# Performance work log

Hardware: AMD Instinct MI355X
Metric: run time of the kernel (lower is better)

Reference implementation:

```python
import jax, jax.numpy as jnp
import numpy as np

B, C, L, D, P = 64, 64, 720, 512, 336
P2, H = P // 2, 512  # H = hidden width of the ProbG branch


def setup_inputs() -> dict:
    key = jax.random.key(0)
    ks = jax.random.split(key, 20)
    def w(k, i, o):
        return jax.random.normal(k, (i, o), jnp.float32) / np.sqrt(i)
    return {
        "x_bsd": jax.random.normal(ks[0], (B, L, C), jnp.float32),
        "z0": jax.random.normal(ks[1], (B, C, D), jnp.float32),
        "y0": jax.random.normal(ks[2], (B, C, P), jnp.float32),
        # ProbG hidden branch (HID_GIVEN_X_V0 -> SS_Z_GIVEN_X_V0)
        "W_h": w(ks[3], L, H),
        "W_ssz": w(ks[4], H, 2 * D),
        # x->z scale/shift flows (versions v2..v5)
        "W_xz_v2": w(ks[5], L, 2 * D),
        "W_xz_v3": w(ks[6], L, 2 * D),
        "W_xz_v4": w(ks[7], L, 2 * D),
        "W_xz_v5": w(ks[8], L, 2 * D),
        # z->x scale/shift flows (v0, v2, v3, v5)
        "W_zx_v0": w(ks[9], D, 2 * L),
        "W_zx_v2": w(ks[10], D, 2 * L),
        "W_zx_v3": w(ks[11], D, 2 * L),
        "W_zx_v5": w(ks[12], D, 2 * L),
        # z->y scale/shift flow (v4, used inside encoding)
        "W_zy_v4": w(ks[13], D, 2 * P),
        # decode heads: ROT_IN_Y_V1 and KOO_Y_GIVEN_Z_V0
        "W_rot": w(ks[14], D, P2),
        "W_koo": w(ks[15], D, 2 * P),
        # Koopman complex params for y-space (a + i b per channel/pair)
        "a_y": jnp.ones((C, P2), jnp.float32),
        "b_y": jnp.zeros((C, P2), jnp.float32) + 0.1,
    }


def _ss(params):
    """Split conditioner output into (positive scale, shift)."""
    s_raw, t = jnp.split(params, 2, axis=-1)
    return jnp.exp(jnp.tanh(s_raw)), t


def _affine(v, cond, W):
    """Scale/shift flow: v <- v * s(cond) + t(cond)."""
    s, t = _ss(jnp.einsum('bck,km->bcm', cond, W))
    return v * s + t


def _rot(u, theta, inv=False):
    """Rotate interleaved (re, im) pairs of u [B,C,P] by angles theta [B,C,P/2]."""
    re, im = u[..., 0::2], u[..., 1::2]
    th = -theta if inv else theta
    c, s = jnp.cos(th), jnp.sin(th)
    return jnp.stack([c * re - s * im, s * re + c * im], axis=-1).reshape(u.shape)


def _koop(u, a, b, inv=False):
    """Koopman unit-complex multiply on interleaved pairs; a,b [C,P/2]."""
    n = jnp.sqrt(a * a + b * b)
    ca, cb = a / n, b / n
    cb = -cb if inv else cb
    re, im = u[..., 0::2], u[..., 1::2]
    return jnp.stack([ca * re - cb * im, cb * re + ca * im], axis=-1).reshape(u.shape)


def reference(x_bsd, z0, y0, W_h, W_ssz, W_xz_v2, W_xz_v3, W_xz_v4, W_xz_v5,
              W_zx_v0, W_zx_v2, W_zx_v3, W_zx_v5, W_zy_v4, W_rot, W_koo, a_y, b_y):
    x = jnp.transpose(x_bsd, (0, 2, 1))  # [B,C,L]
    z = z0 * 0.1                          # [B,C,D]
    y = y0 * 0.1                          # [B,C,P]
    # ---- encoding phase ----
    h = jax.nn.gelu(jnp.einsum('bcl,lk->bck', x, W_h))  # X_to_Z_PROB hidden
    z = _affine(z, h, W_ssz)
    x = _affine(x, z, W_zx_v0)
    z = _affine(z, x, W_xz_v2); x = _affine(x, z, W_zx_v2)
    z = _affine(z, x, W_xz_v3); x = _affine(x, z, W_zx_v3)
    z = _affine(z, x, W_xz_v4); y = _affine(y, z, W_zy_v4)  # Z_to_Y_V4
    z = _affine(z, x, W_xz_v5); x = _affine(x, z, W_zx_v5)
    pre_y = y
    # ---- decode: rotate -> ky -> scale -> ky.inv -> rot.inv -> shift ----
    theta = jnp.pi * jnp.tanh(jnp.einsum('bcd,dp->bcp', z, W_rot))   # [B,C,P/2]
    scale, shift = _ss(jnp.einsum('bcd,dp->bcp', z, W_koo))          # [B,C,P]
    const = _koop(_rot(pre_y, theta), a_y, b_y)
    accu = const * scale
    accu = _rot(_koop(accu, a_y, b_y, inv=True), theta, inv=True) + shift
    return jnp.transpose(accu, (0, 2, 1))  # [B,P,C]
```

## Files before the change

### kernel.cpp

```cpp
#include <hip/hip_runtime.h>
#include <hip/hip_bf16.h>
#include <math.h>

#define BB  64
#define CC  64
#define LL  720
#define LLP 736
#define DD  512
#define PP  336
#define P2C 168
#define HH  512
#define MM  (BB*CC)

typedef _Float16 f16x8 __attribute__((ext_vector_type(8)));
typedef float    f32x4 __attribute__((ext_vector_type(4)));

#define GLDS16(g, l) __builtin_amdgcn_global_load_lds( \
    (const __attribute__((address_space(1))) void*)(g), \
    (__attribute__((address_space(3))) void*)(l), 16, 0, 0)

struct WDesc { const float* src; _Float16* dstHi; _Float16* dstLo;
               int K, N, Kpad, tbase, tilesN; };
struct WTab  { WDesc d[12]; };

__global__ __launch_bounds__(256) void k_convert(WTab tab) {
  __shared__ float tile[16][17];
  const int bid = blockIdx.x;
  int wi = 0;
#pragma unroll
  for (int i = 1; i < 12; ++i) if (bid >= tab.d[i].tbase) wi = i;
  const WDesc d = tab.d[wi];
  const int lt = bid - d.tbase;
  const int tk = lt / d.tilesN, tn = lt % d.tilesN;
  const int k0 = tk * 16, n0 = tn * 16;
  const int tx = threadIdx.x & 15, ty = threadIdx.x >> 4;
  float v = 0.f;
  if (n0 + tx < d.N) v = d.src[(size_t)(k0 + ty) * d.N + n0 + tx];
  tile[ty][tx] = v;
  __syncthreads();
  if (n0 + ty < d.N) {
    const float w = tile[tx][ty];
    const _Float16 h = (_Float16)w;
    const _Float16 l = (_Float16)(w - (float)h);
    const size_t base = (size_t)(n0 + ty) * d.Kpad;
    d.dstHi[base + k0 + tx] = h;
    d.dstLo[base + k0 + tx] = l;
    if (d.Kpad != d.K && k0 + 16 == d.K) {
      d.dstHi[base + d.K + tx] = (_Float16)0.f;
      d.dstLo[base + d.K + tx] = (_Float16)0.f;
    }
  }
}

__global__ __launch_bounds__(256) void k_xpose(const float* __restrict__ xbsd,
                                               _Float16* __restrict__ xhi,
                                               _Float16* __restrict__ xlo) {
  __shared__ float tile[16][17];
  const int b = blockIdx.z, l0 = blockIdx.x * 16, c0 = blockIdx.y * 16;
  const int tx = threadIdx.x, ty = threadIdx.y;
  tile[ty][tx] = xbsd[(size_t)b * LL * CC + (size_t)(l0 + ty) * CC + c0 + tx];
  __syncthreads();
  const float v = tile[tx][ty];
  const _Float16 h = (_Float16)v;
  const _Float16 l = (_Float16)(v - (float)h);
  const size_t m = (size_t)b * CC + c0 + ty;
  xhi[m * LLP + l0 + tx] = h;
  xlo[m * LLP + l0 + tx] = l;
  if (l0 == 704) {
    xhi[m * LLP + 720 + tx] = (_Float16)0.f;
    xlo[m * LLP + 720 + tx] = (_Float16)0.f;
  }
}

template<int EPI, bool DUAL, bool VIN16, bool OUT_T>
__global__ __launch_bounds__(256)
void k_gemm(const _Float16* Ahi, const _Float16* Alo, int lda,
            const _Float16* Whi, const _Float16* Wlo, int ldw,
            const float* Vin32, const _Float16* VinHi,
            const _Float16* VinLo, int ldv, float vscale,
            float* outT32,
            _Float16* outHi, _Float16* outLo, int ldo,
            int Kp, int Nv) {
  constexpr int NB   = DUAL ? 128 : 64;
  constexpr int ABUF = 64 * 32;
  constexpr int BBUF = NB * 32;
  constexpr int NCH  = 8 + 2 * (NB / 16);
  constexpr int NCHW = NCH / 4;
  __shared__ _Float16 smem[2 * ABUF + 2 * BBUF];

  const int m0 = blockIdx.y * 64;
  const int n0 = blockIdx.x * 64;
  const int tid = threadIdx.x;
  const int w = tid >> 6, lane = tid & 63, q = lane >> 4, r = lane & 15;
  const int wr = (w & 1) * 32, wc = (w >> 1) * 32;
  const int lr = lane >> 2, ls = lane & 3;

  f32x4 accS[2][2] = {};
  f32x4 accT[2][2] = {};

  const int nk = Kp >> 5;
  for (int kc = 0; kc < nk; ++kc) {
    const int k0 = kc << 5;
#pragma unroll
    for (int cc = 0; cc < NCHW; ++cc) {
      const int chunk = w * NCHW + cc;
      const _Float16* gsrc;
      _Float16* ldst;
      if (chunk < 4) {
        const int rb = chunk * 16;
        const int R = rb + lr;
        const int ss = ls ^ ((R >> 1) & 3);
        gsrc = Ahi + (size_t)(m0 + R) * lda + k0 + ss * 8;
        ldst = smem + rb * 32;
      } else if (chunk < 8) {
        const int rb = (chunk - 4) * 16;
        const int R = rb + lr;
        const int ss = ls ^ ((R >> 1) & 3);
        gsrc = Alo + (size_t)(m0 + R) * lda + k0 + ss * 8;
        ldst = smem + ABUF + rb * 32;
      } else if (chunk < 8 + NB / 16) {
        const int rb = (chunk - 8) * 16;
        const int R = rb + lr;
        const int ss = ls ^ ((R >> 1) & 3);
        const int wrow = (R < 64) ? (n0 + R) : (Nv + n0 + (R - 64));
        gsrc = Whi + (size_t)wrow * ldw + k0 + ss * 8;
        ldst = smem + 2 * ABUF + rb * 32;
      } else {
        const int rb = (chunk - 8 - NB / 16) * 16;
        const int R = rb + lr;
        const int ss = ls ^ ((R >> 1) & 3);
        const int wrow = (R < 64) ? (n0 + R) : (Nv + n0 + (R - 64));
        gsrc = Wlo + (size_t)wrow * ldw + k0 + ss * 8;
        ldst = smem + 2 * ABUF + BBUF + rb * 32;
      }
      GLDS16(gsrc, ldst);
    }
    __syncthreads();

    f16x8 ah[2], al[2];
#pragma unroll
    for (int rt = 0; rt < 2; ++rt) {
      const int R = wr + rt * 16 + r;
      const int t = (q ^ ((R >> 1) & 3)) * 8;
      ah[rt] = *(const f16x8*)(smem + R * 32 + t);
      al[rt] = *(const f16x8*)(smem + ABUF + R * 32 + t);
    }
#pragma unroll
    for (int ct = 0; ct < 2; ++ct) {
      const int RB = wc + ct * 16 + r;
      const int tb = (q ^ ((RB >> 1) & 3)) * 8;
      const f16x8 bh = *(const f16x8*)(smem + 2 * ABUF + RB * 32 + tb);
      const f16x8 bl = *(const f16x8*)(smem + 2 * ABUF + BBUF + RB * 32 + tb);
#pragma unroll
      for (int rt = 0; rt < 2; ++rt) {
        accS[rt][ct] = __builtin_amdgcn_mfma_f32_16x16x32_f16(ah[rt], bh, accS[rt][ct], 0, 0, 0);
        accS[rt][ct] = __builtin_amdgcn_mfma_f32_16x16x32_f16(al[rt], bh, accS[rt][ct], 0, 0, 0);
        accS[rt][ct] = __builtin_amdgcn_mfma_f32_16x16x32_f16(ah[rt], bl, accS[rt][ct], 0, 0, 0);
      }
      if (DUAL) {
        const int RT = 64 + RB;
        const int tt = (q ^ ((RT >> 1) & 3)) * 8;
        const f16x8 chh = *(const f16x8*)(smem + 2 * ABUF + RT * 32 + tt);
        const f16x8 cll = *(const f16x8*)(smem + 2 * ABUF + BBUF + RT * 32 + tt);
#pragma unroll
        for (int rt = 0; rt < 2; ++rt) {
          accT[rt][ct] = __builtin_amdgcn_mfma_f32_16x16x32_f16(ah[rt], chh, accT[rt][ct], 0, 0, 0);
          accT[rt][ct] = __builtin_amdgcn_mfma_f32_16x16x32_f16(al[rt], chh, accT[rt][ct], 0, 0, 0);
          accT[rt][ct] = __builtin_amdgcn_mfma_f32_16x16x32_f16(ah[rt], cll, accT[rt][ct], 0, 0, 0);
        }
      }
    }
    __syncthreads();
  }

#pragma unroll
  for (int rt = 0; rt < 2; ++rt) {
    const int mb = m0 + wr + rt * 16 + q * 4;
#pragma unroll
    for (int ct = 0; ct < 2; ++ct) {
      const int n = n0 + wc + ct * 16 + r;
      if (n >= Nv) continue;
      if (EPI == 2) {
        *(f32x4*)(outT32 + (size_t)n * MM + mb) = accS[rt][ct];
      } else if (EPI == 1) {
#pragma unroll
        for (int g = 0; g < 4; ++g) {
          const int m = mb + g;
          const float v = accS[rt][ct][g];
          const float o = 0.5f * v * (1.0f + tanhf(0.7978845608028654f * (v + 0.044715f * v * v * v)));
          const _Float16 h = (_Float16)o;
          outHi[(size_t)m * ldo + n] = h;
          outLo[(size_t)m * ldo + n] = (_Float16)(o - (float)h);
        }
      } else {
        f32x4 o;
#pragma unroll
        for (int g = 0; g < 4; ++g) {
          const int m = mb + g;
          float v;
          if (VIN16) {
            v = (float)VinHi[(size_t)m * ldv + n] + (float)VinLo[(size_t)m * ldv + n];
          } else {
            v = Vin32[(size_t)m * ldv + n];
          }
          const float s = expf(tanhf(accS[rt][ct][g]));
          o[g] = v * vscale * s + accT[rt][ct][g];
        }
        if (OUT_T) {
          *(f32x4*)(outT32 + (size_t)n * MM + mb) = o;
        } else {
#pragma unroll
          for (int g = 0; g < 4; ++g) {
            const int m = mb + g;
            const _Float16 h = (_Float16)o[g];
            outHi[(size_t)m * ldo + n] = h;
            outLo[(size_t)m * ldo + n] = (_Float16)(o[g] - (float)h);
          }
        }
      }
    }
  }
}

__global__ __launch_bounds__(256) void k_final(const float* __restrict__ Pt,
                                               const float* __restrict__ yT,
                                               const float* __restrict__ Ay,
                                               const float* __restrict__ By,
                                               float* __restrict__ out) {
  const int c = threadIdx.x;
  const int j = blockIdx.x * 4 + threadIdx.y;
  const int b = blockIdx.y;
  const int m = b * 64 + c;
  const float th = 3.14159265358979323846f * tanhf(Pt[(size_t)j * MM + m]);
  const float sc0 = expf(tanhf(Pt[(size_t)(168 + 2 * j) * MM + m]));
  const float sc1 = expf(tanhf(Pt[(size_t)(169 + 2 * j) * MM + m]));
  const float t0 = Pt[(size_t)(504 + 2 * j) * MM + m];
  const float t1 = Pt[(size_t)(505 + 2 * j) * MM + m];
  const float re = yT[(size_t)(2 * j) * MM + m];
  const float im = yT[(size_t)(2 * j + 1) * MM + m];
  const float a = Ay[c * P2C + j], bb = By[c * P2C + j];
  const float rn = rsqrtf(a * a + bb * bb);
  const float ca = a * rn, cb = bb * rn;
  float s1v, c1;
  sincosf(th, &s1v, &c1);
  const float r1 = c1 * re - s1v * im, i1 = s1v * re + c1 * im;
  const float r2 = ca * r1 - cb * i1,  i2 = cb * r1 + ca * i1;
  const float r3 = r2 * sc0,           i3 = i2 * sc1;
  const float r4 = ca * r3 + cb * i3,  i4 = ca * i3 - cb * r3;
  const float r5 = c1 * r4 + s1v * i4, i5 = c1 * i4 - s1v * r4;
  out[(size_t)b * PP * CC + (size_t)(2 * j) * CC + c]     = r5 + t0;
  out[(size_t)b * PP * CC + (size_t)(2 * j + 1) * CC + c] = i5 + t1;
}

extern "C" void kernel_launch(void* const* d_in, const int* in_sizes, int n_in,
                              void* d_out, int out_size, void* d_ws, size_t ws_size,
                              hipStream_t stream) {
  const float* x_bsd   = (const float*)d_in[0];
  const float* z0      = (const float*)d_in[1];
  const float* y0      = (const float*)d_in[2];
  const float* W_h     = (const float*)d_in[3];
  const float* W_ssz   = (const float*)d_in[4];
  const float* W_xz_v2 = (const float*)d_in[5];
  const float* W_xz_v3 = (const float*)d_in[6];
  const float* W_xz_v4 = (const float*)d_in[7];
  const float* W_xz_v5 = (const float*)d_in[8];
  const float* W_zx_v0 = (const float*)d_in[9];
  const float* W_zx_v2 = (const float*)d_in[10];
  const float* W_zx_v3 = (const float*)d_in[11];
  const float* W_zy_v4 = (const float*)d_in[13];
  const float* W_rot   = (const float*)d_in[14];
  const float* W_koo   = (const float*)d_in[15];
  const float* a_y     = (const float*)d_in[16];
  const float* b_y     = (const float*)d_in[17];
  float* out = (float*)d_out;

  char* p = (char*)d_ws;
  auto alloc = [&](size_t bytes) -> void* {
    void* r = (void*)p; p += (bytes + 255) & ~(size_t)255; return r;
  };
  float*    yT  = (float*)alloc((size_t)PP * MM * 4);
  float*    Pt  = (float*)alloc((size_t)(P2C * 5) * MM * 4);
  _Float16* xhi = (_Float16*)alloc((size_t)MM * LLP * 2);
  _Float16* xlo = (_Float16*)alloc((size_t)MM * LLP * 2);
  _Float16* zhi = (_Float16*)alloc((size_t)MM * DD * 2);
  _Float16* zlo = (_Float16*)alloc((size_t)MM * DD * 2);
  _Float16* hhi = (_Float16*)alloc((size_t)MM * HH * 2);
  _Float16* hlo = (_Float16*)alloc((size_t)MM * HH * 2);
  auto wpair = [&](size_t elems, _Float16** lo) -> _Float16* {
    _Float16* hi = (_Float16*)alloc(elems * 2);
    *lo = (_Float16*)alloc(elems * 2);
    return hi;
  };
  _Float16 *tWhL, *tWsszL, *tWxz2L, *tWxz3L, *tWxz4L, *tWxz5L;
  _Float16 *tWzx0L, *tWzx2L, *tWzx3L, *tWzyL, *tWcatL;
  _Float16* tWh   = wpair((size_t)HH * LLP, &tWhL);
  _Float16* tWssz = wpair((size_t)(2*DD) * DD, &tWsszL);
  _Float16* tWxz2 = wpair((size_t)(2*DD) * LLP, &tWxz2L);
  _Float16* tWxz3 = wpair((size_t)(2*DD) * LLP, &tWxz3L);
  _Float16* tWxz4 = wpair((size_t)(2*DD) * LLP, &tWxz4L);
  _Float16* tWxz5 = wpair((size_t)(2*DD) * LLP, &tWxz5L);
  _Float16* tWzx0 = wpair((size_t)1536 * DD, &tWzx0L);
  _Float16* tWzx2 = wpair((size_t)1536 * DD, &tWzx2L);
  _Float16* tWzx3 = wpair((size_t)1536 * DD, &tWzx3L);
  _Float16* tWzy  = wpair((size_t)768 * DD, &tWzyL);
  _Float16* tWcat = wpair((size_t)896 * DD, &tWcatL);

  WTab tab;
  int base = 0;
  auto put = [&](int i, const float* src, _Float16* dh, _Float16* dl,
                 int K, int N, int Kpad) {
    const int tN = (N + 15) / 16;
    tab.d[i] = WDesc{src, dh, dl, K, N, Kpad, base, tN};
    base += ((K + 15) / 16) * tN;
  };
  put(0,  W_h,     tWh,   tWhL,   LL, HH,   LLP);
  put(1,  W_ssz,   tWssz, tWsszL, DD, 2*DD, DD);
  put(2,  W_xz_v2, tWxz2, tWxz2L, LL, 2*DD, LLP);
  put(3,  W_xz_v3, tWxz3, tWxz3L, LL, 2*DD, LLP);
  put(4,  W_xz_v4, tWxz4, tWxz4L, LL, 2*DD, LLP);
  put(5,  W_xz_v5, tWxz5, tWxz5L, LL, 2*DD, LLP);
  put(6,  W_zx_v0, tWzx0, tWzx0L, DD, 2*LL, DD);
  put(7,  W_zx_v2, tWzx2, tWzx2L, DD, 2*LL, DD);
  put(8,  W_zx_v3, tWzx3, tWzx3L, DD, 2*LL, DD);
  put(9,  W_zy_v4, tWzy,  tWzyL,  DD, 2*PP, DD);
  put(10, W_rot,   tWcat, tWcatL, DD, P2C,  DD);
  put(11, W_koo,   tWcat + (size_t)P2C * DD, tWcatL + (size_t)P2C * DD, DD, 2*PP, DD);
  const int total_tiles = base;

  k_convert<<<dim3(total_tiles), dim3(256), 0, stream>>>(tab);
  k_xpose<<<dim3(45, 4, 64), dim3(16, 16), 0, stream>>>(x_bsd, xhi, xlo);

  const dim3 blk(256);
  k_gemm<1, false, false, false><<<dim3(8, 64), blk, 0, stream>>>(
      xhi, xlo, LLP, tWh, tWhL, LLP,
      nullptr, nullptr, nullptr, 0, 0.f, nullptr, hhi, hlo, HH, LLP, HH);
  k_gemm<0, true, false, false><<<dim3(8, 64), blk, 0, stream>>>(
      hhi, hlo, HH, tWssz, tWsszL, DD,
      z0, nullptr, nullptr, DD, 0.1f, nullptr, zhi, zlo, DD, DD, DD);
  k_gemm<0, true, true, false><<<dim3(12, 64), blk, 0, stream>>>(
      zhi, zlo, DD, tWzx0, tWzx0L, DD,
      nullptr, xhi, xlo, LLP, 1.f, nullptr, xhi, xlo, LLP, DD, LL);
  k_gemm<0, true, true, false><<<dim3(8, 64), blk, 0, stream>>>(
      xhi, xlo, LLP, tWxz2, tWxz2L, LLP,
      nullptr, zhi, zlo, DD, 1.f, nullptr, zhi, zlo, DD, LLP, DD);
  k_gemm<0, true, true, false><<<dim3(12, 64), blk, 0, stream>>>(
      zhi, zlo, DD, tWzx2, tWzx2L, DD,
      nullptr, xhi, xlo, LLP, 1.f, nullptr, xhi, xlo, LLP, DD, LL);
  k_gemm<0, true, true, false><<<dim3(8, 64), blk, 0, stream>>>(
      xhi, xlo, LLP, tWxz3, tWxz3L, LLP,
      nullptr, zhi, zlo, DD, 1.f, nullptr, zhi, zlo, DD, LLP, DD);
  k_gemm<0, true, true, false><<<dim3(12, 64), blk, 0, stream>>>(
      zhi, zlo, DD, tWzx3, tWzx3L, DD,
      nullptr, xhi, xlo, LLP, 1.f, nullptr, xhi, xlo, LLP, DD, LL);
  k_gemm<0, true, true, false><<<dim3(8, 64), blk, 0, stream>>>(
      xhi, xlo, LLP, tWxz4, tWxz4L, LLP,
      nullptr, zhi, zlo, DD, 1.f, nullptr, zhi, zlo, DD, LLP, DD);
  k_gemm<0, true, false, true><<<dim3(6, 64), blk, 0, stream>>>(
      zhi, zlo, DD, tWzy, tWzyL, DD,
      y0, nullptr, nullptr, PP, 0.1f, yT, nullptr, nullptr, 0, DD, PP);
  k_gemm<0, true, true, false><<<dim3(8, 64), blk, 0, stream>>>(
      xhi, xlo, LLP, tWxz5, tWxz5L, LLP,
      nullptr, zhi, zlo, DD, 1.f, nullptr, zhi, zlo, DD, LLP, DD);
  k_gemm<2, false, false, true><<<dim3(14, 64), blk, 0, stream>>>(
      zhi, zlo, DD, tWcat, tWcatL, DD,
      nullptr, nullptr, nullptr, 0, 0.f, Pt, nullptr, nullptr, 0, DD, P2C * 5);
  k_final<<<dim3(42, 64), dim3(64, 4), 0, stream>>>(Pt, yT, a_y, b_y, out);
}
```

Measured before the change: 477.6 us.

## Double-buffer LDS tiles in the MFMA GEMM to overlap loads with compute

Splits shared memory into two stage buffers and prefetches the next K-chunk with global_load_lds while MFMAs consume the current one. This replaces two barriers per K iteration with one. The goal is to hide global-to-LDS latency behind the matrix math. In exchange the LDS footprint doubles, which may reduce the number of resident blocks per CU.

```diff
diff --git a/kernel.cpp b/kernel.cpp
--- a/kernel.cpp
+++ b/kernel.cpp
@@ -84,9 +84,10 @@
   constexpr int NB   = DUAL ? 128 : 64;
   constexpr int ABUF = 64 * 32;
   constexpr int BBUF = NB * 32;
+  constexpr int SBUF = 2 * ABUF + 2 * BBUF;
   constexpr int NCH  = 8 + 2 * (NB / 16);
   constexpr int NCHW = NCH / 4;
-  __shared__ _Float16 smem[2 * ABUF + 2 * BBUF];
+  __shared__ _Float16 smem[2 * SBUF];
 
   const int m0 = blockIdx.y * 64;
   const int n0 = blockIdx.x * 64;
@@ -98,9 +99,9 @@
   f32x4 accS[2][2] = {};
   f32x4 accT[2][2] = {};
 
-  const int nk = Kp >> 5;
-  for (int kc = 0; kc < nk; ++kc) {
+  auto stage = [&](int kc, int bsel) {
     const int k0 = kc << 5;
+    _Float16* sb = smem + bsel * SBUF;
 #pragma unroll
     for (int cc = 0; cc < NCHW; ++cc) {
       const int chunk = w * NCHW + cc;
@@ -111,46 +112,54 @@
         const int R = rb + lr;
         const int ss = ls ^ ((R >> 1) & 3);
         gsrc = Ahi + (size_t)(m0 + R) * lda + k0 + ss * 8;
-        ldst = smem + rb * 32;
+        ldst = sb + rb * 32;
       } else if (chunk < 8) {
         const int rb = (chunk - 4) * 16;
         const int R = rb + lr;
         const int ss = ls ^ ((R >> 1) & 3);
         gsrc = Alo + (size_t)(m0 + R) * lda + k0 + ss * 8;
-        ldst = smem + ABUF + rb * 32;
+        ldst = sb + ABUF + rb * 32;
       } else if (chunk < 8 + NB / 16) {
         const int rb = (chunk - 8) * 16;
         const int R = rb + lr;
         const int ss = ls ^ ((R >> 1) & 3);
         const int wrow = (R < 64) ? (n0 + R) : (Nv + n0 + (R - 64));
         gsrc = Whi + (size_t)wrow * ldw + k0 + ss * 8;
-        ldst = smem + 2 * ABUF + rb * 32;
+        ldst = sb + 2 * ABUF + rb * 32;
       } else {
         const int rb = (chunk - 8 - NB / 16) * 16;
         const int R = rb + lr;
         const int ss = ls ^ ((R >> 1) & 3);
         const int wrow = (R < 64) ? (n0 + R) : (Nv + n0 + (R - 64));
         gsrc = Wlo + (size_t)wrow * ldw + k0 + ss * 8;
-        ldst = smem + 2 * ABUF + BBUF + rb * 32;
+        ldst = sb + 2 * ABUF + BBUF + rb * 32;
       }
       GLDS16(gsrc, ldst);
     }
+  };
+
+  const int nk = Kp >> 5;
+  stage(0, 0);
+  int cur = 0;
+  for (int kc = 0; kc < nk; ++kc) {
     __syncthreads();
+    if (kc + 1 < nk) stage(kc + 1, cur ^ 1);
+    const _Float16* sb = smem + cur * SBUF;
 
     f16x8 ah[2], al[2];
 #pragma unroll
     for (int rt = 0; rt < 2; ++rt) {
       const int R = wr + rt * 16 + r;
       const int t = (q ^ ((R >> 1) & 3)) * 8;
-      ah[rt] = *(const f16x8*)(smem + R * 32 + t);
-      al[rt] = *(const f16x8*)(smem + ABUF + R * 32 + t);
+      ah[rt] = *(const f16x8*)(sb + R * 32 + t);
+      al[rt] = *(const f16x8*)(sb + ABUF + R * 32 + t);
     }
 #pragma unroll
     for (int ct = 0; ct < 2; ++ct) {
       const int RB = wc + ct * 16 + r;
       const int tb = (q ^ ((RB >> 1) & 3)) * 8;
-      const f16x8 bh = *(const f16x8*)(smem + 2 * ABUF + RB * 32 + tb);
-      const f16x8 bl = *(const f16x8*)(smem + 2 * ABUF + BBUF + RB * 32 + tb);
+      const f16x8 bh = *(const f16x8*)(sb + 2 * ABUF + RB * 32 + tb);
+      const f16x8 bl = *(const f16x8*)(sb + 2 * ABUF + BBUF + RB * 32 + tb);
 #pragma unroll
       for (int rt = 0; rt < 2; ++rt) {
         accS[rt][ct] = __builtin_amdgcn_mfma_f32_16x16x32_f16(ah[rt], bh, accS[rt][ct], 0, 0, 0);
@@ -160,8 +169,8 @@
       if (DUAL) {
         const int RT = 64 + RB;
         const int tt = (q ^ ((RT >> 1) & 3)) * 8;
-        const f16x8 chh = *(const f16x8*)(smem + 2 * ABUF + RT * 32 + tt);
-        const f16x8 cll = *(const f16x8*)(smem + 2 * ABUF + BBUF + RT * 32 + tt);
+        const f16x8 chh = *(const f16x8*)(sb + 2 * ABUF + RT * 32 + tt);
+        const f16x8 cll = *(const f16x8*)(sb + 2 * ABUF + BBUF + RT * 32 + tt);
 #pragma unroll
         for (int rt = 0; rt < 2; ++rt) {
           accT[rt][ct] = __builtin_amdgcn_mfma_f32_16x16x32_f16(ah[rt], chh, accT[rt][ct], 0, 0, 0);
@@ -170,7 +179,7 @@
         }
       }
     }
-    __syncthreads();
+    cur ^= 1;
   }
 
 #pragma unroll
```

After: 457.6 us. -4.2%, faster.
